# Kernel optimization log

Measured on AMD Instinct MI355X. Metric: run time of the kernel, lower is better.

## Reference

```python
import jax, jax.numpy as jnp
import numpy as np

B, T, I, H, O = 128, 4096, 64, 256, 64


def setup_inputs() -> dict:
    key = jax.random.key(0)
    ks = jax.random.split(key, 7)
    s_ih = 1.0 / np.sqrt(H)
    return {
        "x": jax.random.normal(ks[0], (B, T, I), dtype=jnp.float32),
        "weight_ih": jax.random.uniform(ks[1], (H, I), minval=-s_ih, maxval=s_ih, dtype=jnp.float32),
        "weight_hh": jax.random.uniform(ks[2], (H, H), minval=-s_ih, maxval=s_ih, dtype=jnp.float32),
        "bias_ih": jax.random.uniform(ks[3], (H,), minval=-s_ih, maxval=s_ih, dtype=jnp.float32),
        "bias_hh": jax.random.uniform(ks[4], (H,), minval=-s_ih, maxval=s_ih, dtype=jnp.float32),
        "weight_y": jax.random.uniform(ks[5], (O, H), minval=-s_ih, maxval=s_ih, dtype=jnp.float32),
        "bias_y": jax.random.uniform(ks[6], (O,), minval=-s_ih, maxval=s_ih, dtype=jnp.float32),
    }


def reference(x, weight_ih, weight_hh, bias_ih, bias_hh, weight_y, bias_y):
    # Precompute input projections for all timesteps in one GEMM: [B,T,H]
    x_proj = jnp.einsum("bti,hi->bth", x, weight_ih) + bias_ih + bias_hh

    def step(h, xp_t):  # h: [B,H], xp_t: [B,H]
        h = jnp.tanh(xp_t + h @ weight_hh.T)
        return h, None

    h0 = jnp.zeros((x.shape[0], weight_hh.shape[0]), dtype=x.dtype)
    h_last, _ = jax.lax.scan(step, h0, jnp.swapaxes(x_proj, 0, 1))  # scan over T
    return h_last @ weight_y.T + bias_y  # [B,O]
```

## Files before the change

### kernel.cpp

```cpp
#include <hip/hip_runtime.h>

typedef _Float16 h2 __attribute__((ext_vector_type(2)));
typedef float f4 __attribute__((ext_vector_type(4)));

static constexpr int NB = 128;
static constexpr int NT = 4096;
static constexpr int NI = 64;
static constexpr int NH = 256;
static constexpr int NO = 64;
static constexpr int CHUNK = 16;

union H2I { int i; h2 h; };

__device__ __forceinline__ float fdot2(h2 a, h2 b, float c) {
#if __has_builtin(__builtin_amdgcn_fdot2)
    return __builtin_amdgcn_fdot2(a, b, c, false);
#else
    return c + (float)a[0] * (float)b[0] + (float)a[1] * (float)b[1];
#endif
}

__device__ __forceinline__ int pack2(float a, float b) {
    H2I u;
    u.h[0] = (_Float16)a;
    u.h[1] = (_Float16)b;
    return u.i;
}
__device__ __forceinline__ h2 toh2(int v) { H2I u; u.i = v; return u.h; }

__device__ __forceinline__ float red_xor8(float v) {
#if __has_builtin(__builtin_amdgcn_mov_dpp)
    int o = __builtin_amdgcn_mov_dpp(__float_as_int(v), 0x128, 0xF, 0xF, true);
    return v + __int_as_float(o);
#else
    return v + __shfl_xor(v, 8, 64);
#endif
}
__device__ __forceinline__ float red_xor16(float v) {
#if __has_builtin(__builtin_amdgcn_ds_swizzle)
    int o = __builtin_amdgcn_ds_swizzle(__float_as_int(v), 0x401F);
    return v + __int_as_float(o);
#else
    return v + __shfl_xor(v, 16, 64);
#endif
}

__device__ __forceinline__ float fast_tanh(float x) {
#if __has_builtin(__builtin_amdgcn_exp2f)
    float e = __builtin_amdgcn_exp2f(x * 2.885390081777927f);
#else
    float e = exp2f(x * 2.885390081777927f);
#endif
#if __has_builtin(__builtin_amdgcn_rcpf)
    return 1.0f - 2.0f * __builtin_amdgcn_rcpf(e + 1.0f);
#else
    return 1.0f - 2.0f / (e + 1.0f);
#endif
}

__global__ __launch_bounds__(256, 1) void rnn_persist(
    const float* __restrict__ x,
    const float* __restrict__ wih,
    const float* __restrict__ whhg,
    const float* __restrict__ bih,
    const float* __restrict__ bhh,
    const float* __restrict__ wy,
    const float* __restrict__ by,
    float* __restrict__ out)
{
    __shared__ int hbuf[2][NH / 2];
    __shared__ int xbuf[2][CHUNK * NI / 2];
    __shared__ float hf[NH];

    const int tid = threadIdx.x;
    const int w = tid >> 6;
    const int l = tid & 63;
    const int r = l & 7;
    const int q = l >> 3;
    const int b5 = l >> 5;
    const bool hi32 = (l >= 32);
    const int b = blockIdx.x;

    h2 whh[8][16];
    h2 wi[8][4];
    const int j0 = 64 * w + 8 * r;
#pragma unroll
    for (int a = 0; a < 8; ++a) {
        const f4* src = (const f4*)(whhg + (size_t)(j0 + a) * NH + 32 * q);
#pragma unroll
        for (int u = 0; u < 8; ++u) {
            f4 v = src[u];
            whh[a][2 * u]     = toh2(pack2(v.x, v.y));
            whh[a][2 * u + 1] = toh2(pack2(v.z, v.w));
        }
        const f4* s2 = (const f4*)(wih + (size_t)(j0 + a) * NI + 8 * q);
#pragma unroll
        for (int u = 0; u < 2; ++u) {
            f4 v = s2[u];
            wi[a][2 * u]     = toh2(pack2(v.x, v.y));
            wi[a][2 * u + 1] = toh2(pack2(v.z, v.w));
        }
    }
    const int jb = j0 + 4 * b5;
    float bias_r[4];
#pragma unroll
    for (int i = 0; i < 4; ++i) bias_r[i] = bih[jb + i] + bhh[jb + i];

    const int sw = q & 3;
    int hoff[4];
#pragma unroll
    for (int c = 0; c < 4; ++c) hoff[c] = 64 * q + 16 * (c ^ sw);
    const int qh = 2 * w + (r >> 2);
    const int pub_off = 64 * qh + 16 * ((r & 3) ^ (qh & 3)) + 8 * b5;
    const bool writer = (l & 24) == 0;

    const float* xb = x + (size_t)b * NT * NI;

    {
        f4 v = ((const f4*)xb)[tid];
        xbuf[0][2 * tid]     = pack2(v.x, v.y);
        xbuf[0][2 * tid + 1] = pack2(v.z, v.w);
    }
    if (tid < NH / 2) hbuf[0][tid] = 0;
    __syncthreads();

    f4 xnext;
    int p = 0;

#pragma unroll 1
    for (int t = 0; t < NT; ++t) {
        const int s = t & (CHUNK - 1);
        const int c = t >> 4;

        if (s == 0 && t + CHUNK < NT) {
            xnext = ((const f4*)(xb + (size_t)(t + CHUNK) * NI))[tid];
        }

        const char* hbp = (const char*)hbuf[p];
        const int4 xv = *(const int4*)((const char*)xbuf[c & 1] + 128 * s + 16 * q);
        const int4 h0 = *(const int4*)(hbp + hoff[0]);
        const int4 h1 = *(const int4*)(hbp + hoff[1]);
        const int4 h2v = *(const int4*)(hbp + hoff[2]);
        const int4 h3 = *(const int4*)(hbp + hoff[3]);

        float acc[8];
#pragma unroll
        for (int a = 0; a < 8; ++a) acc[a] = 0.f;

#pragma unroll
        for (int a = 0; a < 8; ++a) {
            acc[a] = fdot2(wi[a][0], toh2(xv.x), acc[a]);
            acc[a] = fdot2(wi[a][1], toh2(xv.y), acc[a]);
            acc[a] = fdot2(wi[a][2], toh2(xv.z), acc[a]);
            acc[a] = fdot2(wi[a][3], toh2(xv.w), acc[a]);
        }
        const int hc[16] = {h0.x, h0.y, h0.z, h0.w, h1.x, h1.y, h1.z, h1.w,
                            h2v.x, h2v.y, h2v.z, h2v.w, h3.x, h3.y, h3.z, h3.w};
#pragma unroll
        for (int kk = 0; kk < 16; ++kk) {
            const h2 hv = toh2(hc[kk]);
#pragma unroll
            for (int a = 0; a < 8; ++a) acc[a] = fdot2(whh[a][kk], hv, acc[a]);
        }

        float th[4];
#pragma unroll
        for (int i = 0; i < 4; ++i) {
            float cc = hi32 ? acc[i + 4] : acc[i];
            float dd = hi32 ? acc[i] : acc[i + 4];
            cc += __shfl_xor(dd, 32, 64);
            cc = red_xor8(cc);
            cc = red_xor16(cc);
            th[i] = fast_tanh(cc + bias_r[i]);
        }

        if (writer) {
            int2 pk;
            pk.x = pack2(th[0], th[1]);
            pk.y = pack2(th[2], th[3]);
            *(int2*)((char*)hbuf[p ^ 1] + pub_off) = pk;
            if (t == NT - 1) {
                f4 hv;
                hv.x = th[0]; hv.y = th[1]; hv.z = th[2]; hv.w = th[3];
                *(f4*)(&hf[jb]) = hv;
            }
        }

        if (s == CHUNK - 1 && t + 1 < NT) {
            xbuf[(c + 1) & 1][2 * tid]     = pack2(xnext.x, xnext.y);
            xbuf[(c + 1) & 1][2 * tid + 1] = pack2(xnext.z, xnext.w);
        }

        __syncthreads();
        p ^= 1;
    }

    if (tid < NO) {
        float accy = by[tid];
        const f4* wrow = (const f4*)(wy + (size_t)tid * NH);
        const f4* hp = (const f4*)hf;
#pragma unroll
        for (int u = 0; u < NH / 4; ++u) {
            f4 wv = wrow[u];
            f4 hv = hp[u];
            accy += wv.x * hv.x + wv.y * hv.y + wv.z * hv.z + wv.w * hv.w;
        }
        out[b * NO + tid] = accy;
    }
}

extern "C" void kernel_launch(void* const* d_in, const int* in_sizes, int n_in,
                              void* d_out, int out_size, void* d_ws, size_t ws_size,
                              hipStream_t stream) {
    const float* x   = (const float*)d_in[0];
    const float* wih = (const float*)d_in[1];
    const float* whh = (const float*)d_in[2];
    const float* bih = (const float*)d_in[3];
    const float* bhh = (const float*)d_in[4];
    const float* wy  = (const float*)d_in[5];
    const float* by  = (const float*)d_in[6];
    float* out = (float*)d_out;

    rnn_persist<<<dim3(NB), dim3(256), 0, stream>>>(x, wih, whh, bih, bhh, wy, by, out);
}
```

Before: 2.632 ms.

## Precompute input projections in a parallel kernel, stream them into recurrence

Splits the work into a separate kernel that computes the fp16 input projection plus both biases for every timestep into workspace. The recurrent kernel then loads one projected value per output instead of running the input-weight dot products, which shortens the serial per-step critical path. The cross-lane reduction also switches to v_permlane32/16 swap instructions. This costs an extra 256 MB write and read of workspace, and keeps the old fused kernel as a fallback when the workspace is too small.

```diff
diff --git a/kernel.cpp b/kernel.cpp
--- a/kernel.cpp
+++ b/kernel.cpp
@@ -9,6 +9,7 @@
 static constexpr int NH = 256;
 static constexpr int NO = 64;
 static constexpr int CHUNK = 16;
+static constexpr size_t XP_BYTES = (size_t)NB * NT * NH * 2;
 
 union H2I { int i; h2 h; };
 
@@ -36,7 +37,13 @@
     return v + __shfl_xor(v, 8, 64);
 #endif
 }
-__device__ __forceinline__ float red_xor16(float v) {
+__device__ __forceinline__ void swap32(float& a, float& b) {
+    asm("v_permlane32_swap_b32 %0, %1" : "+v"(a), "+v"(b));
+}
+__device__ __forceinline__ void swap16(float& a, float& b) {
+    asm("v_permlane16_swap_b32 %0, %1" : "+v"(a), "+v"(b));
+}
+__device__ __forceinline__ float red_xor16_ds(float v) {
 #if __has_builtin(__builtin_amdgcn_ds_swizzle)
     int o = __builtin_amdgcn_ds_swizzle(__float_as_int(v), 0x401F);
     return v + __int_as_float(o);
@@ -58,18 +65,96 @@
 #endif
 }
 
-__global__ __launch_bounds__(256, 1) void rnn_persist(
-    const float* __restrict__ x,
-    const float* __restrict__ wih,
+__global__ __launch_bounds__(256, 1) void xp_pre(
+    const float* __restrict__ x, const float* __restrict__ wih,
+    const float* __restrict__ bih, const float* __restrict__ bhh,
+    int* __restrict__ xpg)
+{
+    __shared__ int xs[64 * 32];
+    __shared__ int os[64 * 128];
+
+    const int tid = threadIdx.x;
+    const int w = tid >> 6, l = tid & 63;
+    const int b = blockIdx.x >> 1;
+    const int t0 = (blockIdx.x & 1) * (NT / 2);
+
+    h2 wr[4][32];
+    float bs[4];
+#pragma unroll
+    for (int a = 0; a < 4; ++a) {
+        const int j = 4 * l + a;
+        const f4* src = (const f4*)(wih + (size_t)j * NI);
+#pragma unroll
+        for (int u = 0; u < 16; ++u) {
+            f4 v = src[u];
+            wr[a][2 * u]     = toh2(pack2(v.x, v.y));
+            wr[a][2 * u + 1] = toh2(pack2(v.z, v.w));
+        }
+        bs[a] = bih[j] + bhh[j];
+    }
+
+    const float* xbase = x + ((size_t)b * NT + t0) * NI;
+    const int NCH = (NT / 2) / 64;
+
+    f4 ld[4];
+#pragma unroll
+    for (int k = 0; k < 4; ++k) ld[k] = ((const f4*)xbase)[tid * 4 + k];
+
+    for (int ch = 0; ch < NCH; ++ch) {
+        {
+            int4 w0, w1;
+            w0.x = pack2(ld[0].x, ld[0].y); w0.y = pack2(ld[0].z, ld[0].w);
+            w0.z = pack2(ld[1].x, ld[1].y); w0.w = pack2(ld[1].z, ld[1].w);
+            w1.x = pack2(ld[2].x, ld[2].y); w1.y = pack2(ld[2].z, ld[2].w);
+            w1.z = pack2(ld[3].x, ld[3].y); w1.w = pack2(ld[3].z, ld[3].w);
+            *(int4*)&xs[tid * 8] = w0;
+            *(int4*)&xs[tid * 8 + 4] = w1;
+        }
+        __syncthreads();
+        if (ch + 1 < NCH) {
+            const f4* nx = (const f4*)(xbase + (size_t)(ch + 1) * 64 * NI);
+#pragma unroll
+            for (int k = 0; k < 4; ++k) ld[k] = nx[tid * 4 + k];
+        }
+#pragma unroll 1
+        for (int tt = 0; tt < 16; ++tt) {
+            const int tl = tt * 4 + w;
+            const int4* xr = (const int4*)&xs[tl * 32];
+            int4 xv[8];
+#pragma unroll
+            for (int u = 0; u < 8; ++u) xv[u] = xr[u];
+            const int* xd = (const int*)xv;
+            float acc[4] = {0.f, 0.f, 0.f, 0.f};
+#pragma unroll
+            for (int kk = 0; kk < 32; ++kk) {
+                const h2 hv = toh2(xd[kk]);
+#pragma unroll
+                for (int a = 0; a < 4; ++a) acc[a] = fdot2(wr[a][kk], hv, acc[a]);
+            }
+            int2 pk;
+            pk.x = pack2(acc[0] + bs[0], acc[1] + bs[1]);
+            pk.y = pack2(acc[2] + bs[2], acc[3] + bs[3]);
+            *(int2*)&os[tl * 128 + l * 2] = pk;
+        }
+        __syncthreads();
+        {
+            int4* dst = (int4*)xpg + (size_t)(b * NT + t0 + ch * 64) * 32;
+            const int4* s4 = (const int4*)os;
+#pragma unroll
+            for (int k = 0; k < 8; ++k) dst[k * 256 + tid] = s4[k * 256 + tid];
+        }
+        __syncthreads();
+    }
+}
+
+__global__ __launch_bounds__(256, 1) void rnn_rec(
+    const int* __restrict__ xpg,
     const float* __restrict__ whhg,
-    const float* __restrict__ bih,
-    const float* __restrict__ bhh,
-    const float* __restrict__ wy,
-    const float* __restrict__ by,
+    const float* __restrict__ wy, const float* __restrict__ by,
     float* __restrict__ out)
 {
     __shared__ int hbuf[2][NH / 2];
-    __shared__ int xbuf[2][CHUNK * NI / 2];
+    __shared__ int xps[2][CHUNK * NH / 2];
     __shared__ float hf[NH];
 
     const int tid = threadIdx.x;
@@ -78,11 +163,9 @@
     const int r = l & 7;
     const int q = l >> 3;
     const int b5 = l >> 5;
-    const bool hi32 = (l >= 32);
     const int b = blockIdx.x;
 
     h2 whh[8][16];
-    h2 wi[8][4];
     const int j0 = 64 * w + 8 * r;
 #pragma unroll
     for (int a = 0; a < 8; ++a) {
@@ -93,18 +176,8 @@
             whh[a][2 * u]     = toh2(pack2(v.x, v.y));
             whh[a][2 * u + 1] = toh2(pack2(v.z, v.w));
         }
-        const f4* s2 = (const f4*)(wih + (size_t)(j0 + a) * NI + 8 * q);
-#pragma unroll
-        for (int u = 0; u < 2; ++u) {
-            f4 v = s2[u];
-            wi[a][2 * u]     = toh2(pack2(v.x, v.y));
-            wi[a][2 * u + 1] = toh2(pack2(v.z, v.w));
-        }
     }
     const int jb = j0 + 4 * b5;
-    float bias_r[4];
-#pragma unroll
-    for (int i = 0; i < 4; ++i) bias_r[i] = bih[jb + i] + bhh[jb + i];
 
     const int sw = q & 3;
     int hoff[4];
@@ -114,17 +187,16 @@
     const int pub_off = 64 * qh + 16 * ((r & 3) ^ (qh & 3)) + 8 * b5;
     const bool writer = (l & 24) == 0;
 
-    const float* xb = x + (size_t)b * NT * NI;
-
     {
-        f4 v = ((const f4*)xb)[tid];
-        xbuf[0][2 * tid]     = pack2(v.x, v.y);
-        xbuf[0][2 * tid + 1] = pack2(v.z, v.w);
+        const int4* g4 = (const int4*)xpg;
+        const size_t base4 = (size_t)b * NT * 32;
+        *(int4*)&xps[0][tid * 4]        = g4[base4 + tid];
+        *(int4*)&xps[0][tid * 4 + 1024] = g4[base4 + tid + 256];
     }
     if (tid < NH / 2) hbuf[0][tid] = 0;
     __syncthreads();
 
-    f4 xnext;
+    int4 xq0, xq1;
     int p = 0;
 
 #pragma unroll 1
@@ -133,27 +205,23 @@
         const int c = t >> 4;
 
         if (s == 0 && t + CHUNK < NT) {
-            xnext = ((const f4*)(xb + (size_t)(t + CHUNK) * NI))[tid];
+            const int4* g4 = (const int4*)xpg;
+            const size_t base4 = ((size_t)b * NT + t + CHUNK) * 32;
+            xq0 = g4[base4 + tid];
+            xq1 = g4[base4 + tid + 256];
         }
 
         const char* hbp = (const char*)hbuf[p];
-        const int4 xv = *(const int4*)((const char*)xbuf[c & 1] + 128 * s + 16 * q);
         const int4 h0 = *(const int4*)(hbp + hoff[0]);
         const int4 h1 = *(const int4*)(hbp + hoff[1]);
         const int4 h2v = *(const int4*)(hbp + hoff[2]);
         const int4 h3 = *(const int4*)(hbp + hoff[3]);
+        const int2 hx = *(const int2*)&xps[c & 1][s * 128 + (jb >> 1)];
 
         float acc[8];
 #pragma unroll
         for (int a = 0; a < 8; ++a) acc[a] = 0.f;
 
-#pragma unroll
-        for (int a = 0; a < 8; ++a) {
-            acc[a] = fdot2(wi[a][0], toh2(xv.x), acc[a]);
-            acc[a] = fdot2(wi[a][1], toh2(xv.y), acc[a]);
-            acc[a] = fdot2(wi[a][2], toh2(xv.z), acc[a]);
-            acc[a] = fdot2(wi[a][3], toh2(xv.w), acc[a]);
-        }
         const int hc[16] = {h0.x, h0.y, h0.z, h0.w, h1.x, h1.y, h1.z, h1.w,
                             h2v.x, h2v.y, h2v.z, h2v.w, h3.x, h3.y, h3.z, h3.w};
 #pragma unroll
@@ -163,15 +231,18 @@
             for (int a = 0; a < 8; ++a) acc[a] = fdot2(whh[a][kk], hv, acc[a]);
         }
 
+        const h2 xlo = toh2(hx.x), xhi = toh2(hx.y);
+        const float xpf[4] = {(float)xlo[0], (float)xlo[1], (float)xhi[0], (float)xhi[1]};
         float th[4];
 #pragma unroll
         for (int i = 0; i < 4; ++i) {
-            float cc = hi32 ? acc[i + 4] : acc[i];
-            float dd = hi32 ? acc[i] : acc[i + 4];
-            cc += __shfl_xor(dd, 32, 64);
-            cc = red_xor8(cc);
-            cc = red_xor16(cc);
-            th[i] = fast_tanh(cc + bias_r[i]);
+            float a0 = acc[i], a1 = acc[i + 4];
+            swap32(a0, a1);
+            float s5 = a0 + a1;
+            s5 = red_xor8(s5);
+            float u0 = s5, u1 = s5;
+            swap16(u0, u1);
+            th[i] = fast_tanh((u0 + u1) + xpf[i]);
         }
 
         if (writer) {
@@ -187,10 +258,149 @@
         }
 
         if (s == CHUNK - 1 && t + 1 < NT) {
+            *(int4*)&xps[(c + 1) & 1][tid * 4]        = xq0;
+            *(int4*)&xps[(c + 1) & 1][tid * 4 + 1024] = xq1;
+        }
+
+        __syncthreads();
+        p ^= 1;
+    }
+
+    if (tid < NO) {
+        float accy = by[tid];
+        const f4* wrow = (const f4*)(wy + (size_t)tid * NH);
+        const f4* hp = (const f4*)hf;
+#pragma unroll
+        for (int u = 0; u < NH / 4; ++u) {
+            f4 wv = wrow[u];
+            f4 hv = hp[u];
+            accy += wv.x * hv.x + wv.y * hv.y + wv.z * hv.z + wv.w * hv.w;
+        }
+        out[b * NO + tid] = accy;
+    }
+}
+
+__global__ __launch_bounds__(256, 1) void rnn_persist_fb(
+    const float* __restrict__ x, const float* __restrict__ wih,
+    const float* __restrict__ whhg, const float* __restrict__ bih,
+    const float* __restrict__ bhh, const float* __restrict__ wy,
+    const float* __restrict__ by, float* __restrict__ out)
+{
+    __shared__ int hbuf[2][NH / 2];
+    __shared__ int xbuf[2][CHUNK * NI / 2];
+    __shared__ float hf[NH];
+
+    const int tid = threadIdx.x;
+    const int w = tid >> 6;
+    const int l = tid & 63;
+    const int r = l & 7;
+    const int q = l >> 3;
+    const int b5 = l >> 5;
+    const bool hi32 = (l >= 32);
+    const int b = blockIdx.x;
+
+    h2 whh[8][16];
+    h2 wi[8][4];
+    const int j0 = 64 * w + 8 * r;
+#pragma unroll
+    for (int a = 0; a < 8; ++a) {
+        const f4* src = (const f4*)(whhg + (size_t)(j0 + a) * NH + 32 * q);
+#pragma unroll
+        for (int u = 0; u < 8; ++u) {
+            f4 v = src[u];
+            whh[a][2 * u]     = toh2(pack2(v.x, v.y));
+            whh[a][2 * u + 1] = toh2(pack2(v.z, v.w));
+        }
+        const f4* s2 = (const f4*)(wih + (size_t)(j0 + a) * NI + 8 * q);
+#pragma unroll
+        for (int u = 0; u < 2; ++u) {
+            f4 v = s2[u];
+            wi[a][2 * u]     = toh2(pack2(v.x, v.y));
+            wi[a][2 * u + 1] = toh2(pack2(v.z, v.w));
+        }
+    }
+    const int jb = j0 + 4 * b5;
+    float bias_r[4];
+#pragma unroll
+    for (int i = 0; i < 4; ++i) bias_r[i] = bih[jb + i] + bhh[jb + i];
+
+    const int sw = q & 3;
+    int hoff[4];
+#pragma unroll
+    for (int c = 0; c < 4; ++c) hoff[c] = 64 * q + 16 * (c ^ sw);
+    const int qh = 2 * w + (r >> 2);
+    const int pub_off = 64 * qh + 16 * ((r & 3) ^ (qh & 3)) + 8 * b5;
+    const bool writer = (l & 24) == 0;
+
+    const float* xb = x + (size_t)b * NT * NI;
+    {
+        f4 v = ((const f4*)xb)[tid];
+        xbuf[0][2 * tid]     = pack2(v.x, v.y);
+        xbuf[0][2 * tid + 1] = pack2(v.z, v.w);
+    }
+    if (tid < NH / 2) hbuf[0][tid] = 0;
+    __syncthreads();
+
+    f4 xnext;
+    int p = 0;
+
+#pragma unroll 1
+    for (int t = 0; t < NT; ++t) {
+        const int s = t & (CHUNK - 1);
+        const int c = t >> 4;
+        if (s == 0 && t + CHUNK < NT) {
+            xnext = ((const f4*)(xb + (size_t)(t + CHUNK) * NI))[tid];
+        }
+        const char* hbp = (const char*)hbuf[p];
+        const int4 xv = *(const int4*)((const char*)xbuf[c & 1] + 128 * s + 16 * q);
+        const int4 h0 = *(const int4*)(hbp + hoff[0]);
+        const int4 h1 = *(const int4*)(hbp + hoff[1]);
+        const int4 h2v = *(const int4*)(hbp + hoff[2]);
+        const int4 h3 = *(const int4*)(hbp + hoff[3]);
+
+        float acc[8];
+#pragma unroll
+        for (int a = 0; a < 8; ++a) acc[a] = 0.f;
+#pragma unroll
+        for (int a = 0; a < 8; ++a) {
+            acc[a] = fdot2(wi[a][0], toh2(xv.x), acc[a]);
+            acc[a] = fdot2(wi[a][1], toh2(xv.y), acc[a]);
+            acc[a] = fdot2(wi[a][2], toh2(xv.z), acc[a]);
+            acc[a] = fdot2(wi[a][3], toh2(xv.w), acc[a]);
+        }
+        const int hc[16] = {h0.x, h0.y, h0.z, h0.w, h1.x, h1.y, h1.z, h1.w,
+                            h2v.x, h2v.y, h2v.z, h2v.w, h3.x, h3.y, h3.z, h3.w};
+#pragma unroll
+        for (int kk = 0; kk < 16; ++kk) {
+            const h2 hv = toh2(hc[kk]);
+#pragma unroll
+            for (int a = 0; a < 8; ++a) acc[a] = fdot2(whh[a][kk], hv, acc[a]);
+        }
+        float th[4];
+#pragma unroll
+        for (int i = 0; i < 4; ++i) {
+            float cc = hi32 ? acc[i + 4] : acc[i];
+            float dd = hi32 ? acc[i] : acc[i + 4];
+            cc += __shfl_xor(dd, 32, 64);
+            cc = red_xor8(cc);
+            cc = red_xor16_ds(cc);
+            th[i] = fast_tanh(cc + bias_r[i]);
+        }
+        if (writer) {
+            int2 pk;
+            pk.x = pack2(th[0], th[1]);
+            pk.y = pack2(th[2], th[3]);
+            *(int2*)((char*)hbuf[p ^ 1] + pub_off) = pk;
+            if (t == NT - 1) {
+                f4 hv;
+                hv.x = th[0]; hv.y = th[1]; hv.z = th[2]; hv.w = th[3];
+                *(f4*)(&hf[jb]) = hv;
+            }
+        }
+        if (s == CHUNK - 1 && t + 1 < NT) {
             xbuf[(c + 1) & 1][2 * tid]     = pack2(xnext.x, xnext.y);
             xbuf[(c + 1) & 1][2 * tid + 1] = pack2(xnext.z, xnext.w);
         }
-
         __syncthreads();
         p ^= 1;
     }
@@ -221,5 +431,10 @@
     const float* by  = (const float*)d_in[6];
     float* out = (float*)d_out;
 
-    rnn_persist<<<dim3(NB), dim3(256), 0, stream>>>(x, wih, whh, bih, bhh, wy, by, out);
-}
+    if (ws_size >= XP_BYTES) {
+        xp_pre<<<dim3(256), dim3(256), 0, stream>>>(x, wih, bih, bhh, (int*)d_ws);
+        rnn_rec<<<dim3(NB), dim3(256), 0, stream>>>((const int*)d_ws, whh, wy, by, out);
+    } else {
+        rnn_persist_fb<<<dim3(NB), dim3(256), 0, stream>>>(x, wih, whh, bih, bhh, wy, by, out);
+    }
+}
```

Result: no change. 2.682 ms (+1.9%).
